# Kernel optimization log

Measured on AMD Instinct MI355X. Metric: run time of the kernel, lower is better.

The kernel has to match this reference:

```python
import jax, jax.numpy as jnp
import numpy as np

NEG = -9.0e15


def setup_inputs() -> dict:
    key = jax.random.key(0)
    ks = jax.random.split(key, 8)
    N, D_IN, D_OUT, EMB = 100000, 128, 128, 64
    E, NPE = 50000, 32   # hyperedges, nodes per edge
    U, EPN = 50000, 32   # output nodes, edges per node
    stdv = 1.0 / np.sqrt(D_IN)
    return {
        "x": jax.random.normal(ks[0], (N, D_IN), dtype=jnp.float32),
        "seq": jax.random.randint(ks[1], (E, NPE), 0, N, dtype=jnp.int64),
        "text2emb": jax.random.normal(ks[2], (100, EMB), dtype=jnp.float32),
        "useq": jax.random.randint(ks[3], (U, EPN), 0, E, dtype=jnp.int64),
        "data_idx": jax.random.randint(ks[4], (U,), 0, U, dtype=jnp.int64),
        "weight1": jax.random.uniform(ks[5], (D_IN, D_OUT), jnp.float32, -stdv, stdv),
        "weight2": jax.random.uniform(ks[6], (D_OUT, D_OUT), jnp.float32, -stdv, stdv),
        "weight3": jax.random.uniform(ks[7], (100, EMB), jnp.float32, -stdv, stdv),
    }


def _masked_mean_weights(idx):
    # softmax over a {1, -9e15} mask -> uniform weights over nonzero slots
    logits = jnp.where(idx > 0, jnp.float32(1.0), jnp.float32(NEG))
    return jax.nn.softmax(logits, axis=1)


def reference(x, seq, text2emb, useq, data_idx, weight1, weight2, weight3):
    # text_weight is computed in the original forward but never used
    w3n = weight3 / jnp.linalg.norm(weight3, axis=1, keepdims=True)
    cos = w3n @ w3n.T
    _text_weight = cos.mean(axis=1).mean()  # scalar, unused downstream

    h = x @ weight1                              # [N, D_OUT]
    adj_fea = h[seq]                             # [E, NPE, D_OUT] gather
    w = _masked_mean_weights(seq)                # [E, NPE]
    edge = jnp.einsum("enc,en->ec", adj_fea, w)  # [E, D_OUT]
    # dropout is identity in eval mode
    edge = jax.nn.relu(edge)
    e1 = edge @ weight2                          # [E, D_OUT]

    edge_fea = e1[useq]                          # [U, EPN, D_OUT] gather
    uw = _masked_mean_weights(useq)              # [U, EPN]
    node = jnp.einsum("uec,ue->uc", edge_fea, uw)  # [U, D_OUT]
    return node
```

## Files before the change

### kernel.cpp

```cpp
#include <hip/hip_runtime.h>
#include <hip/hip_bf16.h>

#define N_NODES  100000
#define E_EDGES  50000
#define U_NODES  50000
#define D        128
#define NPE      32

typedef __attribute__((ext_vector_type(8))) short short8;
typedef __attribute__((ext_vector_type(4))) unsigned short u16x4;
typedef __attribute__((ext_vector_type(4))) float f32x4;
typedef __attribute__((ext_vector_type(4))) unsigned int u32x4;

static __device__ __forceinline__ unsigned short f2bf_bits(float f) {
    unsigned u = __float_as_uint(f);
    return (unsigned short)((u + 0x7fffu + ((u >> 16) & 1u)) >> 16);
}

static __device__ __forceinline__ int swz(int row, int bytecol) {
    return row * 256 + ((((bytecol >> 4) ^ (row & 7)) << 4) | (bytecol & 15));
}

__global__ __launch_bounds__(256) void prep(const float* __restrict__ w1,
                                            const float* __restrict__ w2,
                                            const float* __restrict__ x,
                                            unsigned short* __restrict__ wt,
                                            unsigned short* __restrict__ xb,
                                            int n8) {
    if (blockIdx.x < 128) {
        const int t = blockIdx.x * 256 + threadIdx.x;
        const int which = t >> 14;
        const int e = t & 16383;
        const int k = e >> 7, c = e & 127;
        const float* w = which ? w2 : w1;
        wt[which * 16384 + c * 128 + k] = f2bf_bits(w[e]);
        return;
    }
    const int i = (blockIdx.x - 128) * 256 + threadIdx.x;
    if (i >= n8) return;
    const float4 a = ((const float4*)x)[2 * i];
    const float4 b = ((const float4*)x)[2 * i + 1];
    uint4 o;
    o.x = (unsigned)f2bf_bits(a.x) | ((unsigned)f2bf_bits(a.y) << 16);
    o.y = (unsigned)f2bf_bits(a.z) | ((unsigned)f2bf_bits(a.w) << 16);
    o.z = (unsigned)f2bf_bits(b.x) | ((unsigned)f2bf_bits(b.y) << 16);
    o.w = (unsigned)f2bf_bits(b.z) | ((unsigned)f2bf_bits(b.w) << 16);
    ((uint4*)xb)[i] = o;
}

template<int OUT_BF16, int RELU>
__global__ __launch_bounds__(256) void gather_mean4(
        const unsigned short* __restrict__ src, const int* __restrict__ idx,
        void* __restrict__ dst, int M) {
    const int wid = (int)((blockIdx.x * blockDim.x + threadIdx.x) >> 6);
    if (wid >= M) return;
    const int lane = threadIdx.x & 63;
    const int g = lane >> 4;
    const int c = lane & 15;

    int my = 0;
    if (lane < NPE) my = idx[(size_t)wid * NPE + lane];
    const unsigned long long b = __ballot(lane < NPE && my > 0);
    const int count = __popcll(b);
    const float scale = 1.0f / (float)(count > 0 ? count : NPE);
    const bool take_all = (count == 0);

    const unsigned short* base = src + c * 8;
    u32x4 v[8];
    float w[8];
#pragma unroll
    for (int i = 0; i < 8; ++i) {
        const int id = __shfl(my, i * 4 + g);
        w[i] = (take_all || id > 0) ? scale : 0.0f;
        const unsigned short* p = base + (size_t)id * D;
        asm volatile("global_load_dwordx4 %0, %1, off sc0 nt"
                     : "=v"(v[i]) : "v"(p));
    }
    asm volatile("s_waitcnt vmcnt(0)" ::: "memory");
    __builtin_amdgcn_sched_barrier(0);

    float acc[8] = {0.f, 0.f, 0.f, 0.f, 0.f, 0.f, 0.f, 0.f};
#pragma unroll
    for (int i = 0; i < 8; ++i) {
        acc[0] = fmaf(__uint_as_float(v[i].x << 16),         w[i], acc[0]);
        acc[1] = fmaf(__uint_as_float(v[i].x & 0xffff0000u), w[i], acc[1]);
        acc[2] = fmaf(__uint_as_float(v[i].y << 16),         w[i], acc[2]);
        acc[3] = fmaf(__uint_as_float(v[i].y & 0xffff0000u), w[i], acc[3]);
        acc[4] = fmaf(__uint_as_float(v[i].z << 16),         w[i], acc[4]);
        acc[5] = fmaf(__uint_as_float(v[i].z & 0xffff0000u), w[i], acc[5]);
        acc[6] = fmaf(__uint_as_float(v[i].w << 16),         w[i], acc[6]);
        acc[7] = fmaf(__uint_as_float(v[i].w & 0xffff0000u), w[i], acc[7]);
    }

#pragma unroll
    for (int i = 0; i < 8; ++i) {
        acc[i] += __shfl_xor(acc[i], 16);
        acc[i] += __shfl_xor(acc[i], 32);
        if (RELU) acc[i] = fmaxf(acc[i], 0.f);
    }

    if (lane < 16) {
        if (OUT_BF16) {
            uint4 o;
            o.x = (unsigned)f2bf_bits(acc[0]) | ((unsigned)f2bf_bits(acc[1]) << 16);
            o.y = (unsigned)f2bf_bits(acc[2]) | ((unsigned)f2bf_bits(acc[3]) << 16);
            o.z = (unsigned)f2bf_bits(acc[4]) | ((unsigned)f2bf_bits(acc[5]) << 16);
            o.w = (unsigned)f2bf_bits(acc[6]) | ((unsigned)f2bf_bits(acc[7]) << 16);
            *(uint4*)((unsigned short*)dst + (size_t)wid * D + c * 8) = o;
        } else {
            float* dp = (float*)dst + (size_t)wid * D + c * 8;
            *(float4*)dp = make_float4(acc[0], acc[1], acc[2], acc[3]);
            *(float4*)(dp + 4) = make_float4(acc[4], acc[5], acc[6], acc[7]);
        }
    }
}

__global__ __launch_bounds__(256) void gemm12(const unsigned short* __restrict__ gx,
                                              const unsigned short* __restrict__ Wt,
                                              unsigned short* __restrict__ e1, int M) {
    __shared__ unsigned short sW1[128 * 128];
    __shared__ unsigned short sW2[128 * 128];
    __shared__ unsigned short sA[64 * 128];
    const int tid = threadIdx.x;
    const int row0 = blockIdx.x * 64;
    const int nrows = min(64, M - row0);

    {
        const float4* w4 = (const float4*)Wt;
#pragma unroll
        for (int j = 0; j < 8; ++j) {
            const int i = tid + j * 256;
            const int r = i >> 4, cc = (i & 15) * 16;
            *(float4*)((char*)sW1 + swz(r, cc)) = w4[i];
            *(float4*)((char*)sW2 + swz(r, cc)) = w4[2048 + i];
        }
    }
    {
#pragma unroll
        for (int j = 0; j < 4; ++j) {
            const int i = tid + j * 256;
            const int r = i >> 4, cc = (i & 15) * 16;
            int gr = row0 + r; if (gr >= M) gr = M - 1;
            *(float4*)((char*)sA + swz(r, cc)) =
                *(const float4*)&gx[(size_t)gr * D + (i & 15) * 8];
        }
    }
    __syncthreads();

    const int lane = tid & 63;
    const int wv = tid >> 6;
    const int r16 = lane & 15;
    const int hi = lane >> 4;
    const int Ra = wv * 16 + r16;

    short8 af[4];
#pragma unroll
    for (int kt = 0; kt < 4; ++kt)
        af[kt] = *(const short8*)((char*)sA + swz(Ra, kt * 64 + hi * 16));

    f32x4 acc[8];
#pragma unroll
    for (int ct = 0; ct < 8; ++ct) acc[ct] = (f32x4){0.f, 0.f, 0.f, 0.f};
#pragma unroll
    for (int ct = 0; ct < 8; ++ct)
#pragma unroll
        for (int kt = 0; kt < 4; ++kt) {
            const short8 bf = *(const short8*)((char*)sW1 + swz(ct * 16 + r16, kt * 64 + hi * 16));
            acc[ct] = __builtin_amdgcn_mfma_f32_16x16x32_bf16(af[kt], bf, acc[ct], 0, 0, 0);
        }

#pragma unroll
    for (int ct = 0; ct < 8; ++ct)
#pragma unroll
        for (int i = 0; i < 4; ++i)
            *(unsigned short*)((char*)sA + swz(wv * 16 + hi * 4 + i, (ct * 16 + r16) * 2)) =
                f2bf_bits(fmaxf(acc[ct][i], 0.f));

    short8 af2[4];
#pragma unroll
    for (int kt = 0; kt < 4; ++kt)
        af2[kt] = *(const short8*)((char*)sA + swz(Ra, kt * 64 + hi * 16));

    f32x4 acc2[8];
#pragma unroll
    for (int ct = 0; ct < 8; ++ct) acc2[ct] = (f32x4){0.f, 0.f, 0.f, 0.f};
#pragma unroll
    for (int ct = 0; ct < 8; ++ct)
#pragma unroll
        for (int kt = 0; kt < 4; ++kt) {
            const short8 bf = *(const short8*)((char*)sW2 + swz(ct * 16 + r16, kt * 64 + hi * 16));
            acc2[ct] = __builtin_amdgcn_mfma_f32_16x16x32_bf16(af2[kt], bf, acc2[ct], 0, 0, 0);
        }

#pragma unroll
    for (int ct = 0; ct < 8; ++ct)
#pragma unroll
        for (int i = 0; i < 4; ++i)
            *(unsigned short*)((char*)sA + swz(wv * 16 + hi * 4 + i, (ct * 16 + r16) * 2)) =
                f2bf_bits(acc2[ct][i]);
    __syncthreads();

#pragma unroll
    for (int j = 0; j < 4; ++j) {
        const int i = tid + j * 256;
        const int r = i >> 4, cc = i & 15;
        if (r < nrows)
            *(float4*)&e1[(size_t)(row0 + r) * D + cc * 8] =
                *(const float4*)((char*)sA + swz(r, cc * 16));
    }
}

extern "C" void kernel_launch(void* const* d_in, const int* in_sizes, int n_in,
                              void* d_out, int out_size, void* d_ws, size_t ws_size,
                              hipStream_t stream) {
    const float* x    = (const float*)d_in[0];
    const int*   seq  = (const int*)d_in[1];
    const int*   useq = (const int*)d_in[3];
    const float* w1   = (const float*)d_in[5];
    const float* w2   = (const float*)d_in[6];
    float* out = (float*)d_out;

    unsigned short* wt = (unsigned short*)d_ws;
    unsigned short* xb = wt + 2 * 16384;
    unsigned short* gx = xb + (size_t)N_NODES * D;
    unsigned short* e1 = gx + (size_t)E_EDGES * D;

    const int n8 = N_NODES * D / 8;
    prep<<<128 + (n8 + 255) / 256, 256, 0, stream>>>(w1, w2, x, wt, xb, n8);

    gather_mean4<1, 0><<<(E_EDGES * 64) / 256, 256, 0, stream>>>(xb, seq, gx, E_EDGES);

    gemm12<<<(E_EDGES + 63) / 64, 256, 0, stream>>>(gx, wt, e1, E_EDGES);

    gather_mean4<0, 0><<<(U_NODES * 64) / 256, 256, 0, stream>>>(e1, useq, out, U_NODES);
}
```

Measured before the change: 251.1 us.

## Split gathers into column slices so each block touches a cache-resident feature slice

Both gather-mean kernels now process 128 edges per block, restricted to one of eight 16-column slices. Neighbouring blocks therefore read the same narrow column band of the source table, which should improve L2 reuse of the randomly indexed rows. Each pair of lanes now handles one edge and loads its indices with wide nontemporal loads, so the wave-level shuffle and cross-lane reduction are gone. The first gather writes its output in a slice-major layout that the GEMM reads back, which changes the GEMM's load addressing. The cost is 32-byte gathers per row, which may use DRAM bandwidth less efficiently, and longer per-thread serial loops.

```diff
diff --git a/kernel.cpp b/kernel.cpp
--- a/kernel.cpp
+++ b/kernel.cpp
@@ -6,11 +6,13 @@
 #define U_NODES  50000
 #define D        128
 #define NPE      32
+#define NSLICE   8
+#define SLICE_COLS 16
 
 typedef __attribute__((ext_vector_type(8))) short short8;
 typedef __attribute__((ext_vector_type(4))) unsigned short u16x4;
 typedef __attribute__((ext_vector_type(4))) float f32x4;
-typedef __attribute__((ext_vector_type(4))) unsigned int u32x4;
+typedef __attribute__((ext_vector_type(4))) int i32x4;
 
 static __device__ __forceinline__ unsigned short f2bf_bits(float f) {
     unsigned u = __float_as_uint(f);
@@ -19,6 +21,23 @@
 
 static __device__ __forceinline__ int swz(int row, int bytecol) {
     return row * 256 + ((((bytecol >> 4) ^ (row & 7)) << 4) | (bytecol & 15));
+}
+
+static __device__ __forceinline__ void acc8(const uint4 v, float w, float* a) {
+    a[0] = fmaf(__uint_as_float(v.x << 16),         w, a[0]);
+    a[1] = fmaf(__uint_as_float(v.x & 0xffff0000u), w, a[1]);
+    a[2] = fmaf(__uint_as_float(v.y << 16),         w, a[2]);
+    a[3] = fmaf(__uint_as_float(v.y & 0xffff0000u), w, a[3]);
+    a[4] = fmaf(__uint_as_float(v.z << 16),         w, a[4]);
+    a[5] = fmaf(__uint_as_float(v.z & 0xffff0000u), w, a[5]);
+    a[6] = fmaf(__uint_as_float(v.w << 16),         w, a[6]);
+    a[7] = fmaf(__uint_as_float(v.w & 0xffff0000u), w, a[7]);
+}
+static __device__ __forceinline__ void set8(const uint4 v, float* a) {
+    a[0] = __uint_as_float(v.x << 16);  a[1] = __uint_as_float(v.x & 0xffff0000u);
+    a[2] = __uint_as_float(v.y << 16);  a[3] = __uint_as_float(v.y & 0xffff0000u);
+    a[4] = __uint_as_float(v.z << 16);  a[5] = __uint_as_float(v.z & 0xffff0000u);
+    a[6] = __uint_as_float(v.w << 16);  a[7] = __uint_as_float(v.w & 0xffff0000u);
 }
 
 __global__ __launch_bounds__(256) void prep(const float* __restrict__ w1,
@@ -48,74 +67,69 @@
     ((uint4*)xb)[i] = o;
 }
 
-template<int OUT_BF16, int RELU>
-__global__ __launch_bounds__(256) void gather_mean4(
+template<int OUT_BF16>
+__global__ __launch_bounds__(256) void gather_slice(
         const unsigned short* __restrict__ src, const int* __restrict__ idx,
         void* __restrict__ dst, int M) {
-    const int wid = (int)((blockIdx.x * blockDim.x + threadIdx.x) >> 6);
-    if (wid >= M) return;
-    const int lane = threadIdx.x & 63;
-    const int g = lane >> 4;
-    const int c = lane & 15;
-
-    int my = 0;
-    if (lane < NPE) my = idx[(size_t)wid * NPE + lane];
-    const unsigned long long b = __ballot(lane < NPE && my > 0);
-    const int count = __popcll(b);
-    const float scale = 1.0f / (float)(count > 0 ? count : NPE);
-    const bool take_all = (count == 0);
-
-    const unsigned short* base = src + c * 8;
-    u32x4 v[8];
-    float w[8];
-#pragma unroll
-    for (int i = 0; i < 8; ++i) {
-        const int id = __shfl(my, i * 4 + g);
-        w[i] = (take_all || id > 0) ? scale : 0.0f;
-        const unsigned short* p = base + (size_t)id * D;
-        asm volatile("global_load_dwordx4 %0, %1, off sc0 nt"
-                     : "=v"(v[i]) : "v"(p));
-    }
-    asm volatile("s_waitcnt vmcnt(0)" ::: "memory");
-    __builtin_amdgcn_sched_barrier(0);
-
-    float acc[8] = {0.f, 0.f, 0.f, 0.f, 0.f, 0.f, 0.f, 0.f};
-#pragma unroll
-    for (int i = 0; i < 8; ++i) {
-        acc[0] = fmaf(__uint_as_float(v[i].x << 16),         w[i], acc[0]);
-        acc[1] = fmaf(__uint_as_float(v[i].x & 0xffff0000u), w[i], acc[1]);
-        acc[2] = fmaf(__uint_as_float(v[i].y << 16),         w[i], acc[2]);
-        acc[3] = fmaf(__uint_as_float(v[i].y & 0xffff0000u), w[i], acc[3]);
-        acc[4] = fmaf(__uint_as_float(v[i].z << 16),         w[i], acc[4]);
-        acc[5] = fmaf(__uint_as_float(v[i].z & 0xffff0000u), w[i], acc[5]);
-        acc[6] = fmaf(__uint_as_float(v[i].w << 16),         w[i], acc[6]);
-        acc[7] = fmaf(__uint_as_float(v[i].w & 0xffff0000u), w[i], acc[7]);
-    }
-
-#pragma unroll
-    for (int i = 0; i < 8; ++i) {
-        acc[i] += __shfl_xor(acc[i], 16);
-        acc[i] += __shfl_xor(acc[i], 32);
-        if (RELU) acc[i] = fmaxf(acc[i], 0.f);
-    }
-
-    if (lane < 16) {
+    const int b = blockIdx.x;
+    const int slice = b & 7;
+    const int tid = threadIdx.x;
+    const int lane = tid & 63;
+    const int wv = tid >> 6;
+    const int sub = lane & 1;
+    const int e_raw = (b >> 3) * 128 + wv * 32 + (lane >> 1);
+    const int e = min(e_raw, M - 1);
+
+    const i32x4* ib = (const i32x4*)(idx + (size_t)e * NPE + sub * 16);
+    const i32x4 q0 = __builtin_nontemporal_load(ib + 0);
+    const i32x4 q1 = __builtin_nontemporal_load(ib + 1);
+    const i32x4 q2 = __builtin_nontemporal_load(ib + 2);
+    const i32x4 q3 = __builtin_nontemporal_load(ib + 3);
+    int idxr[16];
+    idxr[0]=q0.x;  idxr[1]=q0.y;  idxr[2]=q0.z;  idxr[3]=q0.w;
+    idxr[4]=q1.x;  idxr[5]=q1.y;  idxr[6]=q1.z;  idxr[7]=q1.w;
+    idxr[8]=q2.x;  idxr[9]=q2.y;  idxr[10]=q2.z; idxr[11]=q2.w;
+    idxr[12]=q3.x; idxr[13]=q3.y; idxr[14]=q3.z; idxr[15]=q3.w;
+
+    const unsigned short* sbase = src + slice * SLICE_COLS + sub * 8;
+
+    float acc[8] = {0.f,0.f,0.f,0.f,0.f,0.f,0.f,0.f};
+    int cnt = 0;
+    uint4 vlast = make_uint4(0, 0, 0, 0);
+#pragma unroll
+    for (int j = 0; j < 16; ++j) {
+        const int ia = idxr[j];
+        const int ix = __shfl_xor(ia, 1);
+        const int idJ = (sub == 0) ? ia : ix;
+        const int idK = (sub == 0) ? ix : ia;
+        const uint4 vJ = *(const uint4*)(sbase + (size_t)idJ * D);
+        const uint4 vK = *(const uint4*)(sbase + (size_t)idK * D);
+        cnt += (idJ > 0) + (idK > 0);
+        acc8(vJ, (idJ > 0) ? 1.f : 0.f, acc);
+        acc8(vK, (idK > 0) ? 1.f : 0.f, acc);
+        if (j == 15) vlast = vK;
+    }
+    float scale;
+    if (cnt > 0) scale = 1.f / (float)cnt;
+    else { set8(vlast, acc); scale = 1.f; }
+
+    if (e_raw < M) {
         if (OUT_BF16) {
             uint4 o;
-            o.x = (unsigned)f2bf_bits(acc[0]) | ((unsigned)f2bf_bits(acc[1]) << 16);
-            o.y = (unsigned)f2bf_bits(acc[2]) | ((unsigned)f2bf_bits(acc[3]) << 16);
-            o.z = (unsigned)f2bf_bits(acc[4]) | ((unsigned)f2bf_bits(acc[5]) << 16);
-            o.w = (unsigned)f2bf_bits(acc[6]) | ((unsigned)f2bf_bits(acc[7]) << 16);
-            *(uint4*)((unsigned short*)dst + (size_t)wid * D + c * 8) = o;
+            o.x = (unsigned)f2bf_bits(acc[0]*scale) | ((unsigned)f2bf_bits(acc[1]*scale) << 16);
+            o.y = (unsigned)f2bf_bits(acc[2]*scale) | ((unsigned)f2bf_bits(acc[3]*scale) << 16);
+            o.z = (unsigned)f2bf_bits(acc[4]*scale) | ((unsigned)f2bf_bits(acc[5]*scale) << 16);
+            o.w = (unsigned)f2bf_bits(acc[6]*scale) | ((unsigned)f2bf_bits(acc[7]*scale) << 16);
+            *(uint4*)((unsigned short*)dst + ((size_t)slice * M + e) * SLICE_COLS + sub * 8) = o;
         } else {
-            float* dp = (float*)dst + (size_t)wid * D + c * 8;
-            *(float4*)dp = make_float4(acc[0], acc[1], acc[2], acc[3]);
-            *(float4*)(dp + 4) = make_float4(acc[4], acc[5], acc[6], acc[7]);
-        }
-    }
-}
-
-__global__ __launch_bounds__(256) void gemm12(const unsigned short* __restrict__ gx,
+            float* dp = (float*)dst + (size_t)e * D + slice * SLICE_COLS + sub * 8;
+            *(float4*)dp = make_float4(acc[0]*scale, acc[1]*scale, acc[2]*scale, acc[3]*scale);
+            *(float4*)(dp + 4) = make_float4(acc[4]*scale, acc[5]*scale, acc[6]*scale, acc[7]*scale);
+        }
+    }
+}
+
+__global__ __launch_bounds__(256) void gemm12(const unsigned short* __restrict__ gxs,
                                               const unsigned short* __restrict__ Wt,
                                               unsigned short* __restrict__ e1, int M) {
     __shared__ unsigned short sW1[128 * 128];
@@ -139,10 +153,10 @@
 #pragma unroll
         for (int j = 0; j < 4; ++j) {
             const int i = tid + j * 256;
-            const int r = i >> 4, cc = (i & 15) * 16;
+            const int r = i >> 4, c16 = i & 15;
             int gr = row0 + r; if (gr >= M) gr = M - 1;
-            *(float4*)((char*)sA + swz(r, cc)) =
-                *(const float4*)&gx[(size_t)gr * D + (i & 15) * 8];
+            const float4 v = *(const float4*)&gxs[((size_t)(c16 >> 1) * M + gr) * SLICE_COLS + (c16 & 1) * 8];
+            *(float4*)((char*)sA + swz(r, c16 * 16)) = v;
         }
     }
     __syncthreads();
@@ -220,17 +234,18 @@
     const float* w2   = (const float*)d_in[6];
     float* out = (float*)d_out;
 
-    unsigned short* wt = (unsigned short*)d_ws;
-    unsigned short* xb = wt + 2 * 16384;
-    unsigned short* gx = xb + (size_t)N_NODES * D;
-    unsigned short* e1 = gx + (size_t)E_EDGES * D;
+    unsigned short* wt  = (unsigned short*)d_ws;
+    unsigned short* xb  = wt + 2 * 16384;
+    unsigned short* gxs = xb + (size_t)N_NODES * D;
+    unsigned short* e1  = gxs + (size_t)NSLICE * E_EDGES * SLICE_COLS;
 
     const int n8 = N_NODES * D / 8;
     prep<<<128 + (n8 + 255) / 256, 256, 0, stream>>>(w1, w2, x, wt, xb, n8);
 
-    gather_mean4<1, 0><<<(E_EDGES * 64) / 256, 256, 0, stream>>>(xb, seq, gx, E_EDGES);
-
-    gemm12<<<(E_EDGES + 63) / 64, 256, 0, stream>>>(gx, wt, e1, E_EDGES);
-
-    gather_mean4<0, 0><<<(U_NODES * 64) / 256, 256, 0, stream>>>(e1, useq, out, U_NODES);
-}
+    const int gchunks = (E_EDGES + 127) / 128;
+    gather_slice<1><<<gchunks * NSLICE, 256, 0, stream>>>(xb, seq, gxs, E_EDGES);
+
+    gemm12<<<(E_EDGES + 63) / 64, 256, 0, stream>>>(gxs, wt, e1, E_EDGES);
+
+    gather_slice<0><<<gchunks * NSLICE, 256, 0, stream>>>(e1, useq, out, U_NODES);
+}
```

New measurement: 393.9 us. 1.57x slower.
